# Performance work log

Measured on AMD Instinct MI355X. Metric: run time of the kernel, lower is better.

## Reference

```python
import jax, jax.numpy as jnp
import numpy as np

B, S, DIM, H = 2, 2048, 2048, 16
HD = DIM // H  # 128
ROPE_THETA = 10000.0
NEG = -1e9


def setup_inputs() -> dict:
    key = jax.random.key(0)
    ks = jax.random.split(key, 6)
    x = jax.random.normal(ks[0], (B, S, DIM), dtype=jnp.float32)
    # rotary embedding tables: angle[s, j] = s / theta^(2j/HD), j in [0, HD/2)
    inv_freq = 1.0 / (ROPE_THETA ** (jnp.arange(0, HD, 2, dtype=jnp.float32) / HD))
    angles = jnp.arange(S, dtype=jnp.float32)[:, None] * inv_freq[None, :]  # (S, HD/2)
    freqs_cos = jnp.cos(angles)
    freqs_sin = jnp.sin(angles)
    # causal additive mask (1,1,S,S)
    causal = jnp.tril(jnp.ones((S, S), dtype=jnp.bool_))
    mask = jnp.where(causal, 0.0, NEG).astype(jnp.float32)[None, None]
    sc = 1.0 / np.sqrt(DIM)
    wq = jax.random.normal(ks[1], (DIM, DIM), dtype=jnp.float32) * sc
    wk = jax.random.normal(ks[2], (DIM, DIM), dtype=jnp.float32) * sc
    wv = jax.random.normal(ks[3], (DIM, DIM), dtype=jnp.float32) * sc
    wo = jax.random.normal(ks[4], (DIM, DIM), dtype=jnp.float32) * sc
    return {"x": x, "freqs_cos": freqs_cos, "freqs_sin": freqs_sin,
            "mask": mask, "wq": wq, "wk": wk, "wv": wv, "wo": wo}


def _apply_rope(t, cos, sin):
    # t: (B,S,H,HD); cos/sin: (S, HD/2) -> broadcast (1,S,1,HD/2)
    tr = t[..., ::2]
    ti = t[..., 1::2]
    c = cos[None, :, None, :]
    s = sin[None, :, None, :]
    out_r = tr * c - ti * s
    out_i = tr * s + ti * c
    # interleave back: stack on last axis then flatten -> [r0,i0,r1,i1,...]
    return jnp.stack([out_r, out_i], axis=-1).reshape(t.shape)


def reference(x, freqs_cos, freqs_sin, mask, wq, wk, wv, wo):
    b, s, _ = x.shape
    xq = (x @ wq).reshape(b, s, H, HD)
    xk = (x @ wk).reshape(b, s, H, HD)
    xv = (x @ wv).reshape(b, s, H, HD)
    xq = _apply_rope(xq, freqs_cos, freqs_sin)
    xk = _apply_rope(xk, freqs_cos, freqs_sin)
    # (B,H,S,HD)
    q = jnp.transpose(xq, (0, 2, 1, 3)) * (1.0 / np.sqrt(HD))
    k = jnp.transpose(xk, (0, 2, 1, 3))
    v = jnp.transpose(xv, (0, 2, 1, 3))
    attn = jnp.einsum('bhqd,bhkd->bhqk', q, k) + mask[:, :, :s, :s]
    attn = jax.nn.softmax(attn, axis=-1)
    out = jnp.einsum('bhqk,bhkd->bhqd', attn, v)  # (B,H,S,HD)
    out = jnp.transpose(out, (0, 2, 1, 3)).reshape(b, s, H * HD)
    return out @ wo
```

## Files before the change

### kernel.cpp

```cpp
#include <hip/hip_runtime.h>
#include <hip/hip_bf16.h>
#include <cstdint>
#include <cstddef>

#define BB   2
#define SS   2048
#define DD   2048
#define HH   16
#define HDD  128
#define SEC  8388608
#define NKT  32

typedef unsigned short u16;
typedef __attribute__((ext_vector_type(8))) short short8;
typedef __attribute__((ext_vector_type(4))) float f32x4;

__device__ __forceinline__ u16 f2bf(float f) {
  union { float f; uint32_t u; } v; v.f = f;
  uint32_t r = v.u + 0x7fffu + ((v.u >> 16) & 1u);
  return (u16)(r >> 16);
}
__device__ __forceinline__ float bf2f(u16 b) {
  union { uint32_t u; float f; } v; v.u = ((uint32_t)b) << 16;
  return v.f;
}

__device__ __forceinline__ void gload16(const u16* g, u16* l) {
  __builtin_amdgcn_global_load_lds(
      (__attribute__((address_space(1))) void*)g,
      (__attribute__((address_space(3))) void*)l, 16, 0, 0);
}

__global__ void k_prep(const float* __restrict__ x,
                       const float* __restrict__ w0, const float* __restrict__ w1,
                       const float* __restrict__ w2, const float* __restrict__ w3,
                       u16* __restrict__ xb, u16* __restrict__ wt) {
  const int z = blockIdx.z;
  if (z == 4) {
    const int id = blockIdx.y * 64 + blockIdx.x;
    const int t = threadIdx.y * 32 + threadIdx.x;
    const size_t base = ((size_t)id * 256 + t) * 2;
    const float4* xv = reinterpret_cast<const float4*>(x);
    uint2* ov = reinterpret_cast<uint2*>(xb);
#pragma unroll
    for (int u = 0; u < 2; ++u) {
      const float4 v = xv[base + u];
      uint2 p;
      p.x = (uint32_t)f2bf(v.x) | ((uint32_t)f2bf(v.y) << 16);
      p.y = (uint32_t)f2bf(v.z) | ((uint32_t)f2bf(v.w) << 16);
      ov[base + u] = p;
    }
    return;
  }
  __shared__ float tls[32][33];
  const float* w = (z == 0) ? w0 : (z == 1) ? w1 : (z == 2) ? w2 : w3;
  u16* o = wt + (size_t)z * (DD * DD);
  const int n0 = blockIdx.x * 32, k0 = blockIdx.y * 32;
  const int tx = threadIdx.x, ty = threadIdx.y;
#pragma unroll
  for (int i = 0; i < 32; i += 8)
    tls[ty + i][tx] = w[(size_t)(k0 + ty + i) * DD + n0 + tx];
  __syncthreads();
#pragma unroll
  for (int i = 0; i < 32; i += 8)
    o[(size_t)(n0 + ty + i) * DD + k0 + tx] = f2bf(tls[tx][ty + i]);
}

__global__ __launch_bounds__(512, 2) void k_qkv(const u16* __restrict__ A,
                                                const u16* __restrict__ Bt,
                                                u16* __restrict__ out,
                                                const float* __restrict__ fc,
                                                const float* __restrict__ fs) {
  __shared__ __align__(16) u16 As[2][2][128 * 64];
  __shared__ __align__(16) u16 Bs[2][2][128 * 64];
  const int tid = threadIdx.x;
  const int wave = tid >> 6, lane = tid & 63;
  const int c = lane & 15, g = lane >> 4;
  const int wm = wave >> 2, wn = wave & 3;
  const int x7 = c & 7;
  const int lb = blockIdx.x;
  const int wg = (lb & 7) * 48 + (lb >> 3);
  const int bx = wg / 24, by = wg % 24;
  const int row0 = bx * 256, col0 = by * 256;
  const int lr3 = lane >> 3;
  const int kch = ((lane & 7) ^ lr3) << 3;

  auto stgA = [&](int t, int h) {
    u16* dst = &As[t & 1][h][0];
#pragma unroll
    for (int u = 0; u < 2; ++u)
      gload16(A + (size_t)(row0 + u * 128 + h * 64 + wave * 8 + lr3) * DD + t * 64 + kch,
              dst + (u * 64 + wave * 8) * 64);
  };
  auto stgB = [&](int t, int h) {
    u16* dst = &Bs[t & 1][h][0];
#pragma unroll
    for (int u = 0; u < 2; ++u)
      gload16(Bt + (size_t)(col0 + u * 128 + wm * 64 + h * 32 + wn * 8 + lr3) * DD + t * 64 + kch,
              dst + (u * 64 + wave * 8) * 64);
  };
  auto rdA = [&](const u16* bp, int ip, int ks) {
    return *reinterpret_cast<const short8*>(
        bp + (wm * 64 + ip * 16 + c) * 64 + ((((ks << 2) | g) ^ x7) << 3));
  };
  auto rdB = [&](const u16* bp, int jp, int ks) {
    return *reinterpret_cast<const short8*>(
        bp + (wn * 32 + jp * 16 + c) * 64 + ((((ks << 2) | g) ^ x7) << 3));
  };

  f32x4 acc[8][4] = {};
  auto quad = [&](short8 (&af)[4][2], short8 (&bf)[2][2], int io, int jo) {
    __builtin_amdgcn_s_setprio(1);
#pragma unroll
    for (int ks = 0; ks < 2; ++ks)
#pragma unroll
      for (int ip = 0; ip < 4; ++ip)
#pragma unroll
        for (int jp = 0; jp < 2; ++jp)
          acc[io + ip][jo + jp] = __builtin_amdgcn_mfma_f32_16x16x32_bf16(
              af[ip][ks], bf[jp][ks], acc[io + ip][jo + jp], 0, 0, 0);
    __builtin_amdgcn_s_setprio(0);
  };
  auto bar = [&]() {
    asm volatile("" ::: "memory");
    __builtin_amdgcn_s_barrier();
    asm volatile("" ::: "memory");
  };

  stgA(0, 0); stgB(0, 0); stgB(0, 1); stgA(0, 1);
  stgA(1, 0); stgB(1, 0); stgB(1, 1); stgA(1, 1);
  asm volatile("s_waitcnt vmcnt(8)" ::: "memory");
  bar();

  short8 a[4][2], b0[2][2], b1[2][2];
  for (int t = 0; t < NKT; ++t) {
    const u16* A0p = &As[t & 1][0][0];
    const u16* A1p = &As[t & 1][1][0];
    const u16* B0p = &Bs[t & 1][0][0];
    const u16* B1p = &Bs[t & 1][1][0];
    const bool pf = (t + 2 < NKT);
#pragma unroll
    for (int ip = 0; ip < 4; ++ip)
#pragma unroll
      for (int ks = 0; ks < 2; ++ks)
        a[ip][ks] = rdA(A0p, ip, ks);
#pragma unroll
    for (int jp = 0; jp < 2; ++jp)
#pragma unroll
      for (int ks = 0; ks < 2; ++ks)
        b0[jp][ks] = rdB(B0p, jp, ks);
    quad(a, b0, 0, 0);
    bar();
#pragma unroll
    for (int jp = 0; jp < 2; ++jp)
#pragma unroll
      for (int ks = 0; ks < 2; ++ks)
        b1[jp][ks] = rdB(B1p, jp, ks);
    if (pf) { stgA(t + 2, 0); stgB(t + 2, 0); }
    quad(a, b1, 0, 2);
    bar();
#pragma unroll
    for (int ip = 0; ip < 4; ++ip)
#pragma unroll
      for (int ks = 0; ks < 2; ++ks)
        a[ip][ks] = rdA(A1p, ip, ks);
    if (pf) stgB(t + 2, 1);
    quad(a, b0, 4, 0);
    bar();
    if (pf) stgA(t + 2, 1);
    if (t < NKT - 2)
      asm volatile("s_waitcnt vmcnt(8)" ::: "memory");
    else if (t == NKT - 2)
      asm volatile("s_waitcnt vmcnt(0)" ::: "memory");
    quad(a, b1, 4, 2);
    bar();
  }

  const int which = col0 >> 11;
#pragma unroll
  for (int i = 0; i < 8; ++i) {
    const int mb = row0 + wm * 128 + i * 16 + g * 4;
    const int b_ = mb >> 11, s0_ = mb & (SS - 1);
#pragma unroll
    for (int j = 0; j < 4; ++j) {
      const int n = col0 + wn * 64 + j * 16 + c;
      const int h_ = (n >> 7) & 15, d_ = n & (HDD - 1);
      if (which == 2) {
        ushort4 pk;
        pk.x = f2bf(acc[i][j][0]); pk.y = f2bf(acc[i][j][1]);
        pk.z = f2bf(acc[i][j][2]); pk.w = f2bf(acc[i][j][3]);
        *reinterpret_cast<ushort4*>(
            out + 2 * (size_t)SEC + (((size_t)(b_ * HH + h_)) * HDD + d_) * SS + s0_) = pk;
      } else {
        const int p = d_ >> 1;
        const bool ev = (d_ & 1) == 0;
        const float qsc = (which == 0) ? 0.08838834764831845f : 1.0f;
#pragma unroll
        for (int r = 0; r < 4; ++r) {
          const int s_ = s0_ + r;
          const float own = acc[i][j][r];
          const float par = __shfl_xor(own, 1);
          const float cv = fc[s_ * 64 + p], sv = fs[s_ * 64 + p];
          const float ro = ev ? (own * cv - par * sv) : (par * sv + own * cv);
          out[(size_t)which * SEC + (((size_t)(b_ * HH + h_)) * SS + s_) * HDD + d_] =
              f2bf(ro * qsc);
        }
      }
    }
  }
}

__global__ __launch_bounds__(512, 2) void k_out(const u16* __restrict__ A,
                                                const u16* __restrict__ Bt,
                                                float* __restrict__ out) {
  __shared__ __align__(16) u16 As[2][2][128 * 64];
  __shared__ __align__(16) u16 Bs[2][128 * 64];
  const int tid = threadIdx.x;
  const int wave = tid >> 6, lane = tid & 63;
  const int c = lane & 15, g = lane >> 4;
  const int wm = wave >> 2, wn = wave & 3;
  const int x7 = c & 7;
  const int lb = blockIdx.x;
  const int wg = (lb & 7) * 32 + (lb >> 3);
  const int bx = wg >> 4, by = wg & 15;
  const int row0 = bx * 256, col0 = by * 128;
  const int lr3 = lane >> 3;
  const int kch = ((lane & 7) ^ lr3) << 3;

  auto stgA = [&](int t, int h) {
    u16* dst = &As[t & 1][h][0];
#pragma unroll
    for (int u = 0; u < 2; ++u)
      gload16(A + (size_t)(row0 + u * 128 + h * 64 + wave * 8 + lr3) * DD + t * 64 + kch,
              dst + (u * 64 + wave * 8) * 64);
  };
  auto stgB = [&](int t) {
    u16* dst = &Bs[t & 1][0];
#pragma unroll
    for (int u = 0; u < 2; ++u) {
      const int r0 = u * 64 + wave * 8;
      gload16(Bt + (size_t)(col0 + r0 + lr3) * DD + t * 64 + kch,
              dst + r0 * 64);
    }
  };
  auto rdA = [&](const u16* bp, int ip, int ks) {
    return *reinterpret_cast<const short8*>(
        bp + (wm * 64 + ip * 16 + c) * 64 + ((((ks << 2) | g) ^ x7) << 3));
  };
  auto rdB = [&](const u16* bp, int jp, int ks) {
    return *reinterpret_cast<const short8*>(
        bp + (wn * 32 + jp * 16 + c) * 64 + ((((ks << 2) | g) ^ x7) << 3));
  };

  f32x4 acc[8][2] = {};
  auto quad = [&](short8 (&af)[4][2], short8 (&bf)[2][2], int io) {
    __builtin_amdgcn_s_setprio(1);
#pragma unroll
    for (int ks = 0; ks < 2; ++ks)
#pragma unroll
      for (int ip = 0; ip < 4; ++ip)
#pragma unroll
        for (int jp = 0; jp < 2; ++jp)
          acc[io + ip][jp] = __builtin_amdgcn_mfma_f32_16x16x32_bf16(
              af[ip][ks], bf[jp][ks], acc[io + ip][jp], 0, 0, 0);
    __builtin_amdgcn_s_setprio(0);
  };
  auto bar = [&]() {
    asm volatile("" ::: "memory");
    __builtin_amdgcn_s_barrier();
    asm volatile("" ::: "memory");
  };

  stgA(0, 0); stgB(0);
  stgA(0, 1);
  stgA(1, 0); stgB(1);
  asm volatile("s_waitcnt vmcnt(6)" ::: "memory");
  bar();

  short8 a[4][2], b[2][2];
  for (int t = 0; t < NKT; ++t) {
    const u16* A0p = &As[t & 1][0][0];
    const u16* A1p = &As[t & 1][1][0];
    const u16* Bp  = &Bs[t & 1][0];
    if (t + 1 < NKT) stgA(t + 1, 1);
#pragma unroll
    for (int ip = 0; ip < 4; ++ip)
#pragma unroll
      for (int ks = 0; ks < 2; ++ks)
        a[ip][ks] = rdA(A0p, ip, ks);
#pragma unroll
    for (int jp = 0; jp < 2; ++jp)
#pragma unroll
      for (int ks = 0; ks < 2; ++ks)
        b[jp][ks] = rdB(Bp, jp, ks);
    quad(a, b, 0);
    if (t < NKT - 1)
      asm volatile("s_waitcnt vmcnt(6)" ::: "memory");
    else
      asm volatile("s_waitcnt vmcnt(0)" ::: "memory");
    bar();
    if (t + 2 < NKT) { stgA(t + 2, 0); stgB(t + 2); }
#pragma unroll
    for (int ip = 0; ip < 4; ++ip)
#pragma unroll
      for (int ks = 0; ks < 2; ++ks)
        a[ip][ks] = rdA(A1p, ip, ks);
    quad(a, b, 4);
    if (t < NKT - 2)
      asm volatile("s_waitcnt vmcnt(6)" ::: "memory");
    else if (t == NKT - 2)
      asm volatile("s_waitcnt vmcnt(2)" ::: "memory");
    bar();
  }

#pragma unroll
  for (int i = 0; i < 8; ++i) {
    const int mb = row0 + wm * 128 + i * 16 + g * 4;
#pragma unroll
    for (int j = 0; j < 2; ++j) {
      const int n = col0 + wn * 32 + j * 16 + c;
#pragma unroll
      for (int r = 0; r < 4; ++r)
        out[(size_t)(mb + r) * DD + n] = acc[i][j][r];
    }
  }
}

__global__ __launch_bounds__(256, 3) void k_attn(const u16* __restrict__ Q,
                                                 const u16* __restrict__ K,
                                                 const u16* __restrict__ Vt,
                                                 u16* __restrict__ O) {
  __shared__ __align__(16) u16 Kt[2][32 * 128];
  __shared__ __align__(16) u16 Vs[2][128 * 32];
  __shared__ __align__(16) u16 Pb[4 * 32 * 40];
  const int tid = threadIdx.x;
  const int wave = tid >> 6, lane = tid & 63;
  const int c = lane & 15, g = lane >> 4;
  const int l = blockIdx.x;
  int qi, bh;
  if (l < 256) { qi = 8 + (l & 7); bh = l >> 3; }
  else         { qi = 7 - ((l - 256) & 7); bh = (l - 256) >> 3; }
  const int q0 = qi * 128;
  const u16* Qp = Q  + (size_t)bh * SS * HDD;
  const u16* Kp = K  + (size_t)bh * SS * HDD;
  const u16* Vp = Vt + (size_t)bh * SS * HDD;
  short8 qf[2][4];
#pragma unroll
  for (int ms = 0; ms < 2; ++ms)
#pragma unroll
    for (int kd = 0; kd < 4; ++kd)
      qf[ms][kd] = *reinterpret_cast<const short8*>(
          Qp + (size_t)(q0 + wave * 32 + ms * 16 + c) * HDD + kd * 32 + g * 8);
  f32x4 acc[2][8] = {};
  float psum[2][4] = {};
  const int ntiles = (qi + 1) * 4;
  u16* pwav = Pb + wave * (32 * 40);
  const int krl = lane >> 4, kcl = lane & 15;
  const int vrl = lane >> 2, vcl = lane & 3;
  auto stage = [&](int t) {
    const int kv0 = t * 32;
    u16* kb = Kt[t & 1];
    u16* vb = Vs[t & 1];
#pragma unroll
    for (int j = 0; j < 2; ++j) {
      const int r0k = (j * 4 + wave) * 4;
      const int rowk = r0k + krl;
      gload16(Kp + (size_t)(kv0 + rowk) * HDD + ((kcl ^ (rowk & 15)) << 3),
              kb + r0k * 128);
      const int r0v = (j * 4 + wave) * 16;
      const int rowv = r0v + vrl;
      gload16(Vp + (size_t)rowv * SS + kv0 + ((vcl ^ (vrl & 3)) << 3),
              vb + r0v * 32);
    }
  };
  stage(0);
  for (int t = 0; t < ntiles; ++t) {
    __syncthreads();
    if (t + 1 < ntiles) stage(t + 1);
    const int kv0 = t * 32;
    const bool active = kv0 <= q0 + wave * 32 + 31;
    if (!active) continue;
    const u16* kb = Kt[t & 1];
    const u16* vv = Vs[t & 1];
    f32x4 s[2][2] = {};
#pragma unroll
    for (int ns = 0; ns < 2; ++ns)
#pragma unroll
      for (int kd = 0; kd < 4; ++kd) {
        const short8 b = *reinterpret_cast<const short8*>(
            kb + (ns * 16 + c) * 128 + (((kd * 4 + g) ^ c) << 3));
        s[0][ns] = __builtin_amdgcn_mfma_f32_16x16x32_bf16(qf[0][kd], b, s[0][ns], 0, 0, 0);
        s[1][ns] = __builtin_amdgcn_mfma_f32_16x16x32_bf16(qf[1][kd], b, s[1][ns], 0, 0, 0);
      }
#pragma unroll
    for (int ms = 0; ms < 2; ++ms) {
      const int qrow = q0 + wave * 32 + ms * 16 + g * 4;
#pragma unroll
      for (int r = 0; r < 4; ++r) {
        u16* pw = pwav + (ms * 16 + g * 4 + r) * 40 + c;
        float rs = 0.f;
#pragma unroll
        for (int ns = 0; ns < 2; ++ns) {
          const bool u = (kv0 + ns * 16 + c) <= (qrow + r);
          const float p = u ? __expf(s[ms][ns][r]) : 0.f;
          rs += p;
          pw[ns * 16] = f2bf(p);
        }
        psum[ms][r] += rs;
      }
    }
    short8 pa[2];
    pa[0] = *reinterpret_cast<const short8*>(pwav + c * 40 + g * 8);
    pa[1] = *reinterpret_cast<const short8*>(pwav + (16 + c) * 40 + g * 8);
#pragma unroll
    for (int nb = 0; nb < 8; ++nb) {
      const short8 vb2 = *reinterpret_cast<const short8*>(
          vv + (nb * 16 + c) * 32 + ((g ^ (c & 3)) << 3));
      acc[0][nb] = __builtin_amdgcn_mfma_f32_16x16x32_bf16(pa[0], vb2, acc[0][nb], 0, 0, 0);
      acc[1][nb] = __builtin_amdgcn_mfma_f32_16x16x32_bf16(pa[1], vb2, acc[1][nb], 0, 0, 0);
    }
  }
  const int b_ = bh >> 4, h_ = bh & 15;
#pragma unroll
  for (int ms = 0; ms < 2; ++ms) {
#pragma unroll
    for (int r = 0; r < 4; ++r) {
      float rs = psum[ms][r];
      rs += __shfl_xor(rs, 1);
      rs += __shfl_xor(rs, 2);
      rs += __shfl_xor(rs, 4);
      rs += __shfl_xor(rs, 8);
      const float inv = 1.f / rs;
      const int s_ = q0 + wave * 32 + ms * 16 + g * 4 + r;
      u16* op = O + ((size_t)(b_ * SS + s_)) * DD + h_ * HDD;
#pragma unroll
      for (int nb = 0; nb < 8; ++nb)
        op[nb * 16 + c] = f2bf(acc[ms][nb][r] * inv);
    }
  }
}

extern "C" void kernel_launch(void* const* d_in, const int* in_sizes, int n_in,
                              void* d_out, int out_size, void* d_ws, size_t ws_size,
                              hipStream_t stream) {
  const float* x  = (const float*)d_in[0];
  const float* fc = (const float*)d_in[1];
  const float* fs = (const float*)d_in[2];
  const float* wq = (const float*)d_in[4];
  const float* wk = (const float*)d_in[5];
  const float* wv = (const float*)d_in[6];
  const float* wo = (const float*)d_in[7];

  u16* ws  = (u16*)d_ws;
  u16* xb  = ws;
  u16* wqt = xb  + 8388608;
  u16* wot = wqt + 3 * 4194304;
  u16* Qb  = wot + 4194304;
  u16* Kb  = Qb  + SEC;
  u16* Vtb = Kb  + SEC;
  u16* ao  = Vtb + SEC;

  k_prep<<<dim3(64, 64, 5), dim3(32, 8), 0, stream>>>(x, wq, wk, wv, wo, xb, wqt);
  k_qkv<<<384, 512, 0, stream>>>(xb, wqt, Qb, fc, fs);
  k_attn<<<512, 256, 0, stream>>>(Qb, Kb, Vtb, ao);
  k_out<<<256, 512, 0, stream>>>(ao, wot, (float*)d_out);
}
```

Before: 425.8 us.

## Split-K output projection with larger tiles and vectorize weight transpose prep

The output projection now uses 256x256 tiles with K split in two halves across blocks. Each half writes fp32 partials into dead workspace regions, and a new reduction kernel adds them into the output. The weight-transpose prep kernel now uses 64x64 tiles with float4 loads and 16-byte packed bf16 stores, and the x conversion is spread across more grid slices. This raises operand reuse in the GEMM but adds an extra pass of partial-sum writes and reads plus another launch.

```diff
diff --git a/kernel.cpp b/kernel.cpp
--- a/kernel.cpp
+++ b/kernel.cpp
@@ -36,9 +36,9 @@
                        const float* __restrict__ w2, const float* __restrict__ w3,
                        u16* __restrict__ xb, u16* __restrict__ wt) {
   const int z = blockIdx.z;
-  if (z == 4) {
-    const int id = blockIdx.y * 64 + blockIdx.x;
-    const int t = threadIdx.y * 32 + threadIdx.x;
+  const int t = threadIdx.y * 32 + threadIdx.x;
+  if (z >= 4) {
+    const int id = (z - 4) * 1024 + blockIdx.y * 32 + blockIdx.x;
     const size_t base = ((size_t)id * 256 + t) * 2;
     const float4* xv = reinterpret_cast<const float4*>(x);
     uint2* ov = reinterpret_cast<uint2*>(xb);
@@ -52,18 +52,34 @@
     }
     return;
   }
-  __shared__ float tls[32][33];
+  __shared__ float tls[64][65];
   const float* w = (z == 0) ? w0 : (z == 1) ? w1 : (z == 2) ? w2 : w3;
   u16* o = wt + (size_t)z * (DD * DD);
-  const int n0 = blockIdx.x * 32, k0 = blockIdx.y * 32;
-  const int tx = threadIdx.x, ty = threadIdx.y;
-#pragma unroll
-  for (int i = 0; i < 32; i += 8)
-    tls[ty + i][tx] = w[(size_t)(k0 + ty + i) * DD + n0 + tx];
+  const int n0 = blockIdx.x * 64, k0 = blockIdx.y * 64;
+#pragma unroll
+  for (int i = 0; i < 4; ++i) {
+    const int f = t + 256 * i;
+    const int row = f >> 4, c4 = (f & 15) << 2;
+    const float4 v = *reinterpret_cast<const float4*>(
+        w + (size_t)(k0 + row) * DD + n0 + c4);
+    tls[row][c4 + 0] = v.x; tls[row][c4 + 1] = v.y;
+    tls[row][c4 + 2] = v.z; tls[row][c4 + 3] = v.w;
+  }
   __syncthreads();
 #pragma unroll
-  for (int i = 0; i < 32; i += 8)
-    o[(size_t)(n0 + ty + i) * DD + k0 + tx] = f2bf(tls[tx][ty + i]);
+  for (int i = 0; i < 2; ++i) {
+    const int nrow = (t >> 3) + 32 * i;
+    const int kc8 = (t & 7) << 3;
+    uint32_t pk[4];
+#pragma unroll
+    for (int jj = 0; jj < 4; ++jj) {
+      const uint32_t lo = f2bf(tls[kc8 + 2 * jj][nrow]);
+      const uint32_t hi = f2bf(tls[kc8 + 2 * jj + 1][nrow]);
+      pk[jj] = lo | (hi << 16);
+    }
+    *reinterpret_cast<uint4*>(o + (size_t)(n0 + nrow) * DD + k0 + kc8) =
+        make_uint4(pk[0], pk[1], pk[2], pk[3]);
+  }
 }
 
 __global__ __launch_bounds__(512, 2) void k_qkv(const u16* __restrict__ A,
@@ -210,11 +226,13 @@
   }
 }
 
-__global__ __launch_bounds__(512, 2) void k_out(const u16* __restrict__ A,
-                                                const u16* __restrict__ Bt,
-                                                float* __restrict__ out) {
+#define NKT2 16
+__global__ __launch_bounds__(512, 2) void k_outp(const u16* __restrict__ A,
+                                                 const u16* __restrict__ Bt,
+                                                 float* __restrict__ p0,
+                                                 float* __restrict__ p1) {
   __shared__ __align__(16) u16 As[2][2][128 * 64];
-  __shared__ __align__(16) u16 Bs[2][128 * 64];
+  __shared__ __align__(16) u16 Bs[2][2][128 * 64];
   const int tid = threadIdx.x;
   const int wave = tid >> 6, lane = tid & 63;
   const int c = lane & 15, g = lane >> 4;
@@ -222,8 +240,12 @@
   const int x7 = c & 7;
   const int lb = blockIdx.x;
   const int wg = (lb & 7) * 32 + (lb >> 3);
-  const int bx = wg >> 4, by = wg & 15;
-  const int row0 = bx * 256, col0 = by * 128;
+  const int bx = wg >> 4;
+  const int by = (wg >> 1) & 7;
+  const int ks_ = wg & 1;
+  const int row0 = bx * 256, col0 = by * 256;
+  const int kb0 = ks_ * (DD / 2);
+  float* part = ks_ ? p1 : p0;
   const int lr3 = lane >> 3;
   const int kch = ((lane & 7) ^ lr3) << 3;
 
@@ -231,17 +253,15 @@
     u16* dst = &As[t & 1][h][0];
 #pragma unroll
     for (int u = 0; u < 2; ++u)
-      gload16(A + (size_t)(row0 + u * 128 + h * 64 + wave * 8 + lr3) * DD + t * 64 + kch,
+      gload16(A + (size_t)(row0 + u * 128 + h * 64 + wave * 8 + lr3) * DD + kb0 + t * 64 + kch,
               dst + (u * 64 + wave * 8) * 64);
   };
-  auto stgB = [&](int t) {
-    u16* dst = &Bs[t & 1][0];
-#pragma unroll
-    for (int u = 0; u < 2; ++u) {
-      const int r0 = u * 64 + wave * 8;
-      gload16(Bt + (size_t)(col0 + r0 + lr3) * DD + t * 64 + kch,
-              dst + r0 * 64);
-    }
+  auto stgB = [&](int t, int h) {
+    u16* dst = &Bs[t & 1][h][0];
+#pragma unroll
+    for (int u = 0; u < 2; ++u)
+      gload16(Bt + (size_t)(col0 + u * 128 + wm * 64 + h * 32 + wn * 8 + lr3) * DD + kb0 + t * 64 + kch,
+              dst + (u * 64 + wave * 8) * 64);
   };
   auto rdA = [&](const u16* bp, int ip, int ks) {
     return *reinterpret_cast<const short8*>(
@@ -252,8 +272,8 @@
         bp + (wn * 32 + jp * 16 + c) * 64 + ((((ks << 2) | g) ^ x7) << 3));
   };
 
-  f32x4 acc[8][2] = {};
-  auto quad = [&](short8 (&af)[4][2], short8 (&bf)[2][2], int io) {
+  f32x4 acc[8][4] = {};
+  auto quad = [&](short8 (&af)[4][2], short8 (&bf)[2][2], int io, int jo) {
     __builtin_amdgcn_s_setprio(1);
 #pragma unroll
     for (int ks = 0; ks < 2; ++ks)
@@ -261,8 +281,8 @@
       for (int ip = 0; ip < 4; ++ip)
 #pragma unroll
         for (int jp = 0; jp < 2; ++jp)
-          acc[io + ip][jp] = __builtin_amdgcn_mfma_f32_16x16x32_bf16(
-              af[ip][ks], bf[jp][ks], acc[io + ip][jp], 0, 0, 0);
+          acc[io + ip][jo + jp] = __builtin_amdgcn_mfma_f32_16x16x32_bf16(
+              af[ip][ks], bf[jp][ks], acc[io + ip][jo + jp], 0, 0, 0);
     __builtin_amdgcn_s_setprio(0);
   };
   auto bar = [&]() {
@@ -271,18 +291,18 @@
     asm volatile("" ::: "memory");
   };
 
-  stgA(0, 0); stgB(0);
-  stgA(0, 1);
-  stgA(1, 0); stgB(1);
-  asm volatile("s_waitcnt vmcnt(6)" ::: "memory");
+  stgA(0, 0); stgB(0, 0); stgB(0, 1); stgA(0, 1);
+  stgA(1, 0); stgB(1, 0); stgB(1, 1); stgA(1, 1);
+  asm volatile("s_waitcnt vmcnt(8)" ::: "memory");
   bar();
 
-  short8 a[4][2], b[2][2];
-  for (int t = 0; t < NKT; ++t) {
+  short8 a[4][2], b0[2][2], b1[2][2];
+  for (int t = 0; t < NKT2; ++t) {
     const u16* A0p = &As[t & 1][0][0];
     const u16* A1p = &As[t & 1][1][0];
-    const u16* Bp  = &Bs[t & 1][0];
-    if (t + 1 < NKT) stgA(t + 1, 1);
+    const u16* B0p = &Bs[t & 1][0][0];
+    const u16* B1p = &Bs[t & 1][1][0];
+    const bool pf = (t + 2 < NKT2);
 #pragma unroll
     for (int ip = 0; ip < 4; ++ip)
 #pragma unroll
@@ -292,24 +312,31 @@
     for (int jp = 0; jp < 2; ++jp)
 #pragma unroll
       for (int ks = 0; ks < 2; ++ks)
-        b[jp][ks] = rdB(Bp, jp, ks);
-    quad(a, b, 0);
-    if (t < NKT - 1)
-      asm volatile("s_waitcnt vmcnt(6)" ::: "memory");
-    else
+        b0[jp][ks] = rdB(B0p, jp, ks);
+    quad(a, b0, 0, 0);
+    bar();
+#pragma unroll
+    for (int jp = 0; jp < 2; ++jp)
+#pragma unroll
+      for (int ks = 0; ks < 2; ++ks)
+        b1[jp][ks] = rdB(B1p, jp, ks);
+    if (pf) { stgA(t + 2, 0); stgB(t + 2, 0); }
+    quad(a, b1, 0, 2);
+    bar();
+#pragma unroll
+    for (int ip = 0; ip < 4; ++ip)
+#pragma unroll
+      for (int ks = 0; ks < 2; ++ks)
+        a[ip][ks] = rdA(A1p, ip, ks);
+    if (pf) stgB(t + 2, 1);
+    quad(a, b0, 4, 0);
+    bar();
+    if (pf) stgA(t + 2, 1);
+    if (t < NKT2 - 2)
+      asm volatile("s_waitcnt vmcnt(8)" ::: "memory");
+    else if (t == NKT2 - 2)
       asm volatile("s_waitcnt vmcnt(0)" ::: "memory");
-    bar();
-    if (t + 2 < NKT) { stgA(t + 2, 0); stgB(t + 2); }
-#pragma unroll
-    for (int ip = 0; ip < 4; ++ip)
-#pragma unroll
-      for (int ks = 0; ks < 2; ++ks)
-        a[ip][ks] = rdA(A1p, ip, ks);
-    quad(a, b, 4);
-    if (t < NKT - 2)
-      asm volatile("s_waitcnt vmcnt(6)" ::: "memory");
-    else if (t == NKT - 2)
-      asm volatile("s_waitcnt vmcnt(2)" ::: "memory");
+    quad(a, b1, 4, 2);
     bar();
   }
 
@@ -317,12 +344,23 @@
   for (int i = 0; i < 8; ++i) {
     const int mb = row0 + wm * 128 + i * 16 + g * 4;
 #pragma unroll
-    for (int j = 0; j < 2; ++j) {
-      const int n = col0 + wn * 32 + j * 16 + c;
+    for (int j = 0; j < 4; ++j) {
+      const int n = col0 + wn * 64 + j * 16 + c;
 #pragma unroll
       for (int r = 0; r < 4; ++r)
-        out[(size_t)(mb + r) * DD + n] = acc[i][j][r];
-    }
+        part[(size_t)(mb + r) * DD + n] = acc[i][j][r];
+    }
+  }
+}
+
+__global__ __launch_bounds__(256) void k_red(const float4* __restrict__ p0,
+                                             const float4* __restrict__ p1,
+                                             float4* __restrict__ o) {
+  const size_t i = ((size_t)blockIdx.x * 256 + threadIdx.x) * 2;
+#pragma unroll
+  for (int u = 0; u < 2; ++u) {
+    const float4 a = p0[i + u], b = p1[i + u];
+    o[i + u] = make_float4(a.x + b.x, a.y + b.y, a.z + b.z, a.w + b.w);
   }
 }
 
@@ -459,9 +497,13 @@
   u16* Kb  = Qb  + SEC;
   u16* Vtb = Kb  + SEC;
   u16* ao  = Vtb + SEC;
-
-  k_prep<<<dim3(64, 64, 5), dim3(32, 8), 0, stream>>>(x, wq, wk, wv, wo, xb, wqt);
+  float* p0 = (float*)Qb;
+  float* p1 = (float*)xb;
+
+  k_prep<<<dim3(32, 32, 8), dim3(32, 8), 0, stream>>>(x, wq, wk, wv, wo, xb, wqt);
   k_qkv<<<384, 512, 0, stream>>>(xb, wqt, Qb, fc, fs);
   k_attn<<<512, 256, 0, stream>>>(Qb, Kb, Vtb, ao);
-  k_out<<<256, 512, 0, stream>>>(ao, wot, (float*)d_out);
-}
+  k_outp<<<256, 512, 0, stream>>>(ao, wot, p0, p1);
+  k_red<<<4096, 256, 0, stream>>>((const float4*)p0, (const float4*)p1,
+                                  (float4*)d_out);
+}
```

Result: no change. 420.6 us (-1.2%).
